# Optimization experiments

Measured on AMD Instinct MI355X. Metric: run time of the kernel, lower is better.

The kernel has to match this reference:

```python
import jax, jax.numpy as jnp
import numpy as np

B = 64
T0_V = 512   # existing timesteps already in the graph memory
TAU_V = 128  # new timesteps inserted this call
NTOT = T0_V + TAU_V  # 640 == graph_size
FEAT = 256
K = 16       # causal temporal window (edges j->i for j in [i-K, i))


def _build_edges():
    # per-batch causal edges, then offset by b*NTOT into the flat graph
    src_l, dst_l = [], []
    for off in range(1, K + 1):
        ii = np.arange(off, NTOT)
        src_l.append(ii - off)
        dst_l.append(ii)
    src = np.concatenate(src_l)
    dst = np.concatenate(dst_l)
    boff = (np.arange(B) * NTOT)[:, None]
    edge_src = (src[None, :] + boff).reshape(-1)
    edge_dst = (dst[None, :] + boff).reshape(-1)
    return jnp.asarray(edge_src, jnp.int32), jnp.asarray(edge_dst, jnp.int32)


def setup_inputs() -> dict:
    key = jax.random.key(0)
    ks = jax.random.split(key, 8)
    x = jax.random.normal(ks[0], (B, TAU_V, FEAT), jnp.float32)
    nodes = 0.1 * jax.random.normal(ks[1], (B, NTOT, FEAT), jnp.float32)
    edge_src, edge_dst = _build_edges()
    E = edge_src.shape[0]
    edge_weight = jnp.ones((E,), jnp.float32)
    sc = 1.0 / np.sqrt(FEAT)
    W1_self = sc * jax.random.normal(ks[2], (FEAT, FEAT), jnp.float32)
    W1_nbr = sc * jax.random.normal(ks[3], (FEAT, FEAT), jnp.float32)
    b1 = jnp.zeros((FEAT,), jnp.float32)
    W2_self = sc * jax.random.normal(ks[4], (FEAT, FEAT), jnp.float32)
    W2_nbr = sc * jax.random.normal(ks[5], (FEAT, FEAT), jnp.float32)
    b2 = jnp.zeros((FEAT,), jnp.float32)
    return {"x": x, "nodes": nodes, "edge_weight": edge_weight,
            "W1_self": W1_self, "W1_nbr": W1_nbr, "b1": b1,
            "W2_self": W2_self, "W2_nbr": W2_nbr, "b2": b2,
            "edge_src": edge_src, "edge_dst": edge_dst,
            "T0": T0_V, "tau": TAU_V}


def reference(x, nodes, edge_weight, W1_self, W1_nbr, b1, W2_self, W2_nbr, b2,
              edge_src, edge_dst, T0, tau):
    Bv, t, feat = x.shape
    ntot = T0 + tau
    # scatter new observations into the node memory (uniform taus -> dense slice)
    nodes = nodes.at[:, T0:T0 + tau, :].set(x)
    # adj normalization: values / values.detach() == 1 in the forward pass
    w = edge_weight / jax.lax.stop_gradient(edge_weight)
    # flatten per-batch ragged graphs (regular here since taus are uniform)
    flat = nodes[:, :ntot].reshape(Bv * ntot, feat)  # [B*ntot, feat]
    nseg = Bv * ntot

    def gconv(h, Ws, Wn, b):
        msg = h[edge_src] * w[:, None]                       # [E, d] gather
        agg = jax.ops.segment_sum(msg, edge_dst, num_segments=nseg)
        return jnp.tanh(h @ Ws + agg @ Wn + b)

    h = gconv(flat, W1_self, W1_nbr, b1)
    h = gconv(h, W2_self, W2_nbr, b2)
    # gather outputs for the newly-inserted nodes -> [B, tau, out_feat]
    out_idx = (jnp.arange(Bv)[:, None] * ntot + T0 + jnp.arange(tau)[None, :]).reshape(-1)
    mx_dense = h[out_idx].reshape(Bv, tau, -1)
    return mx_dense
```

## Files before the change

### kernel.cpp

```cpp
#include <hip/hip_runtime.h>
#include <hip/hip_bf16.h>


namespace {

constexpr int BQ    = 64;
constexpr int FEATC = 256;
constexpr int M1 = 144;
constexpr int M2 = 128;

using ushort = unsigned short;
using short8 = __attribute__((ext_vector_type(8))) short;
using f32x4  = __attribute__((ext_vector_type(4))) float;

__device__ __forceinline__ ushort f2bf(float f) {
  union { float f; unsigned u; } v{f};
  unsigned r = v.u + 0x7FFFu + ((v.u >> 16) & 1u);
  return (ushort)(r >> 16);
}
__device__ __forceinline__ float bf2f(ushort h) {
  union { unsigned u; float f; } v{(unsigned)h << 16};
  return v.f;
}
__device__ __forceinline__ void split2(float v, ushort& hi, ushort& lo) {
  hi = f2bf(v);
  lo = f2bf(v - bf2f(hi));
}
__device__ __forceinline__ float tanh_fast(float x) {
  const float e = __builtin_amdgcn_exp2f(x * 2.8853900817779268f);
  return 1.0f - 2.0f * __builtin_amdgcn_rcpf(1.0f + e);
}

__device__ __forceinline__ size_t frag_idx(int row, int k, int s) {
  return ((size_t)(((row >> 4) * 16 + (k >> 5)) * 2 + s)) * 512
       + ((k >> 3) & 3) * 128 + (row & 15) * 8 + (k & 7);
}
__device__ __forceinline__ int lofs(int row_l, int k, int s) {
  return ((k >> 5) * 2 + s) * 512 + ((k >> 3) & 3) * 128 + row_l * 8 + (k & 7);
}

__global__ __launch_bounds__(256) void prep_fused(
    const float* __restrict__ x, const float* __restrict__ nodes,
    const float* __restrict__ W1s, const float* __restrict__ W1n,
    const float* __restrict__ W2s, const float* __restrict__ W2n,
    ushort* __restrict__ A1F, ushort* __restrict__ WF1,
    ushort* __restrict__ WF2) {
  __shared__ ushort lds_o[16384];
  __shared__ float tile[64][65];
  const int blk = blockIdx.x;
  if (blk < 576) {
    const int G = 4 * (blk % 144) + (blk / 144);
    const int b = G / 9, c = G % 9, f = threadIdx.x;
    const int t0 = c * 16, i0 = 496 + t0;
    const float* nb = nodes + ((size_t)b * 640) * FEATC + f;
    const float* xb = x     + ((size_t)b * 128) * FEATC + f;

    float v[32];
    #pragma unroll
    for (int d = 0; d < 32; ++d) {
      const int i = i0 - 16 + d;
      v[d] = (i < 512) ? nb[(size_t)i * FEATC] : xb[(size_t)(i - 512) * FEATC];
    }
    float win = 0.f;
    #pragma unroll
    for (int d = 0; d < 16; ++d) win += v[d];

    #pragma unroll
    for (int tt = 0; tt < 16; ++tt) {
      ushort hi, lo;
      split2(v[16 + tt], hi, lo);
      lds_o[lofs(tt, f, 0)] = hi;
      lds_o[lofs(tt, f, 1)] = lo;
      split2(win, hi, lo);
      lds_o[lofs(tt, 256 + f, 0)] = hi;
      lds_o[lofs(tt, 256 + f, 1)] = lo;
      win += v[16 + tt] - v[tt];
    }
    __syncthreads();
    ushort* dst = A1F + (size_t)G * 16384;
    #pragma unroll
    for (int it = 0; it < 8; ++it) {
      const int idx = it * 256 + threadIdx.x;
      *(short8*)(dst + idx * 8) = *(const short8*)(lds_o + idx * 8);
    }
  } else {
    const int w = blk - 576;
    const int z = w >> 4, rem = w & 15;
    const int k0 = (rem >> 2) * 64, n0 = (rem & 3) * 64;
    const float* src = (z == 0) ? W1s : (z == 1) ? W1n : (z == 2) ? W2s : W2n;
    ushort* dst = (z < 2) ? WF1 : WF2;
    const int koff = (z & 1) * 256;
    const int c = threadIdx.x & 63, r4 = threadIdx.x >> 6;
    #pragma unroll
    for (int p = 0; p < 16; ++p) {
      const int k = r4 + p * 4;
      tile[k][c] = src[(size_t)(k0 + k) * FEATC + n0 + c];
    }
    __syncthreads();
    #pragma unroll
    for (int p = 0; p < 16; ++p) {
      const int n = r4 + p * 4;
      ushort hi, lo;
      split2(tile[c][n], hi, lo);
      dst[frag_idx(n0 + n, koff + k0 + c, 0)] = hi;
      dst[frag_idx(n0 + n, koff + k0 + c, 1)] = lo;
    }
  }
}

#define GLOAD(dst, ptr)                                                      \
  asm volatile("global_load_dwordx4 %0, %1, off"                             \
               : "=v"(dst) : "v"(ptr) : "memory")

#define WAITV(n) do {                                                        \
  asm volatile("s_waitcnt vmcnt(" #n ")" ::: "memory");                      \
  __builtin_amdgcn_sched_barrier(0);                                         \
} while (0)

#define MF(a, b, c) c = __builtin_amdgcn_mfma_f32_16x16x32_bf16(a, b, c, 0, 0, 0)

struct FJ { short8 a0h, a0l, a1h, a1l, a2h, a2l, a3h, a3l, a4h, a4l, wh, wl; };

#define LOADJ(Q, kb) do {                                                    \
  GLOAD(Q.a0h, bA0 + (kb) * 1024); GLOAD(Q.a0l, bA0 + (kb) * 1024 + 512);    \
  GLOAD(Q.a1h, bA1 + (kb) * 1024); GLOAD(Q.a1l, bA1 + (kb) * 1024 + 512);    \
  GLOAD(Q.a2h, bA2 + (kb) * 1024); GLOAD(Q.a2l, bA2 + (kb) * 1024 + 512);    \
  GLOAD(Q.a3h, bA3 + (kb) * 1024); GLOAD(Q.a3l, bA3 + (kb) * 1024 + 512);    \
  GLOAD(Q.a4h, bA4 + (kb) * 1024); GLOAD(Q.a4l, bA4 + (kb) * 1024 + 512);    \
  GLOAD(Q.wh,  bW  + (kb) * 1024); GLOAD(Q.wl,  bW  + (kb) * 1024 + 512);    \
} while (0)

#define COMPJ(Q) do {                                                        \
  __builtin_amdgcn_s_setprio(1);                                             \
  MF(Q.a0h, Q.wh, acc[0]); MF(Q.a1h, Q.wh, acc[1]); MF(Q.a2h, Q.wh, acc[2]); \
  MF(Q.a3h, Q.wh, acc[3]); MF(Q.a4h, Q.wh, acc[4]);                          \
  MF(Q.a0h, Q.wl, acc[0]); MF(Q.a1h, Q.wl, acc[1]); MF(Q.a2h, Q.wl, acc[2]); \
  MF(Q.a3h, Q.wl, acc[3]); MF(Q.a4h, Q.wl, acc[4]);                          \
  MF(Q.a0l, Q.wh, acc[0]); MF(Q.a1l, Q.wh, acc[1]); MF(Q.a2l, Q.wh, acc[2]); \
  MF(Q.a3l, Q.wh, acc[3]); MF(Q.a4l, Q.wh, acc[4]);                          \
  __builtin_amdgcn_s_setprio(0);                                             \
  __builtin_amdgcn_sched_barrier(0);                                         \
} while (0)

__global__ __launch_bounds__(256, 2) void gemm1_fused(
    const ushort* __restrict__ A, const ushort* __restrict__ W,
    const float* __restrict__ bias, ushort* __restrict__ A2F) {
  __shared__ float hvt[80][68];
  __shared__ ushort outb[16384];

  const int tid = threadIdx.x;
  const int wave = tid >> 6, lane = tid & 63;
  const int lr = lane & 15, kg = lane >> 4;
  const int mx2 = blockIdx.x, ny = blockIdx.y;
  const int b = mx2 >> 1, half = mx2 & 1;
  const int rgA0 = 9 * b + 4 * half;
  const int n0 = ny * 64;
  const int ngw = ny * 4 + wave;

  const ushort* bA0 = A + (size_t)(rgA0 + 0) * 16384 + lane * 8;
  const ushort* bA1 = A + (size_t)(rgA0 + 1) * 16384 + lane * 8;
  const ushort* bA2 = A + (size_t)(rgA0 + 2) * 16384 + lane * 8;
  const ushort* bA3 = A + (size_t)(rgA0 + 3) * 16384 + lane * 8;
  const ushort* bA4 = A + (size_t)(rgA0 + 4) * 16384 + lane * 8;
  const ushort* bW  = W + (size_t)ngw * 16384 + lane * 8;

  f32x4 acc[5] = {};
  FJ q0, q1, q2, q3;

  LOADJ(q0, 0); LOADJ(q1, 1); LOADJ(q2, 2); LOADJ(q3, 3);
  WAITV(36); COMPJ(q0); LOADJ(q0, 4);
  WAITV(36); COMPJ(q1); LOADJ(q1, 5);
  WAITV(36); COMPJ(q2); LOADJ(q2, 6);
  WAITV(36); COMPJ(q3); LOADJ(q3, 7);
  WAITV(36); COMPJ(q0); LOADJ(q0, 8);
  WAITV(36); COMPJ(q1); LOADJ(q1, 9);
  WAITV(36); COMPJ(q2); LOADJ(q2, 10);
  WAITV(36); COMPJ(q3); LOADJ(q3, 11);
  WAITV(36); COMPJ(q0); LOADJ(q0, 12);
  WAITV(36); COMPJ(q1); LOADJ(q1, 13);
  WAITV(36); COMPJ(q2); LOADJ(q2, 14);
  WAITV(36); COMPJ(q3); LOADJ(q3, 15);
  WAITV(36); COMPJ(q0);
  WAITV(24); COMPJ(q1);
  WAITV(12); COMPJ(q2);
  WAITV(0);  COMPJ(q3);

  const float bv = bias[n0 + wave * 16 + lr];
  #pragma unroll
  for (int fr = 0; fr < 5; ++fr)
    #pragma unroll
    for (int r = 0; r < 4; ++r)
      hvt[fr * 16 + kg * 4 + r][wave * 16 + lr] = tanh_fast(acc[fr][r] + bv);
  __syncthreads();

  {
    const int col = tid & 63, q = tid >> 6;
    float hv[32];
    #pragma unroll
    for (int d = 0; d < 32; ++d) hv[d] = hvt[q * 16 + d][col];
    float win = 0.f;
    #pragma unroll
    for (int d = 0; d < 16; ++d) win += hv[d];

    const int su = ((q * 4 + (col >> 5)) * 2) * 512
                 + ((col >> 3) & 3) * 128 + (col & 7);
    const int wu = ((q * 4 + 2 + (col >> 5)) * 2) * 512
                 + ((col >> 3) & 3) * 128 + (col & 7);
    #pragma unroll
    for (int tt = 0; tt < 16; ++tt) {
      ushort hi, lo;
      split2(hv[16 + tt], hi, lo);
      outb[su + tt * 8]       = hi;
      outb[su + tt * 8 + 512] = lo;
      split2(win, hi, lo);
      outb[wu + tt * 8]       = hi;
      outb[wu + tt * 8 + 512] = lo;
      win += hv[16 + tt] - hv[tt];
    }
  }
  __syncthreads();

  const int rg20 = 4 * mx2;
  #pragma unroll
  for (int it = 0; it < 8; ++it) {
    const int lin = it * 2048 + tid * 8;
    const int u = lin >> 9, w = lin & 511;
    const int uq = u >> 3, ukbl = (u >> 1) & 3, us = u & 1;
    const int KB = (ukbl < 2) ? (2 * ny + ukbl) : (8 + 2 * ny + (ukbl - 2));
    const size_t dst = ((size_t)((rg20 + uq) * 16 + KB) * 2 + us) * 512 + w;
    *(short8*)(A2F + dst) = *(const short8*)(outb + lin);
  }
}

struct FB { short8 ah0, ah1, al0, al1, b10, b11, b20, b21; };

#define LOADI(Q, tt) do {                                                    \
  GLOAD(Q.ah0, baseA00 + (tt) * 1024);                                       \
  GLOAD(Q.ah1, baseA10 + (tt) * 1024);                                       \
  GLOAD(Q.al0, baseA01 + (tt) * 1024);                                       \
  GLOAD(Q.al1, baseA11 + (tt) * 1024);                                       \
  GLOAD(Q.b10, baseW0h + (tt) * 1024);                                       \
  GLOAD(Q.b11, baseW1h + (tt) * 1024);                                       \
  GLOAD(Q.b20, baseW0l + (tt) * 1024);                                       \
  GLOAD(Q.b21, baseW1l + (tt) * 1024);                                       \
} while (0)

#define COMP(Q) do {                                                         \
  __builtin_amdgcn_s_setprio(1);                                             \
  MF(Q.ah0, Q.b10, acc00); MF(Q.ah0, Q.b11, acc01);                          \
  MF(Q.ah1, Q.b10, acc10); MF(Q.ah1, Q.b11, acc11);                          \
  MF(Q.ah0, Q.b20, acc00); MF(Q.ah0, Q.b21, acc01);                          \
  MF(Q.ah1, Q.b20, acc10); MF(Q.ah1, Q.b21, acc11);                          \
  MF(Q.al0, Q.b10, acc00); MF(Q.al0, Q.b11, acc01);                          \
  MF(Q.al1, Q.b10, acc10); MF(Q.al1, Q.b11, acc11);                          \
  __builtin_amdgcn_s_setprio(0);                                             \
  __builtin_amdgcn_sched_barrier(0);                                         \
} while (0)

__global__ __launch_bounds__(256, 2) void gemm_mfma(
    const ushort* __restrict__ A, const ushort* __restrict__ W,
    const float* __restrict__ bias, float* __restrict__ out) {
  const int t = threadIdx.x;
  const int wave = t >> 6, lane = t & 63;
  const int lr = lane & 15, kg = lane >> 4;
  const int m0 = blockIdx.x * 64 + (wave >> 1) * 32;
  const int n0 = blockIdx.y * 64 + (wave & 1) * 32;
  const int rg0 = m0 >> 4, ng0 = n0 >> 4;

  const ushort* baseA00 = A + ((size_t)((rg0 + 0) * 32 + 0)) * 512 + lane * 8;
  const ushort* baseA01 = A + ((size_t)((rg0 + 0) * 32 + 1)) * 512 + lane * 8;
  const ushort* baseA10 = A + ((size_t)((rg0 + 1) * 32 + 0)) * 512 + lane * 8;
  const ushort* baseA11 = A + ((size_t)((rg0 + 1) * 32 + 1)) * 512 + lane * 8;
  const ushort* baseW0h = W + ((size_t)((ng0 + 0) * 32 + 0)) * 512 + lane * 8;
  const ushort* baseW0l = W + ((size_t)((ng0 + 0) * 32 + 1)) * 512 + lane * 8;
  const ushort* baseW1h = W + ((size_t)((ng0 + 1) * 32 + 0)) * 512 + lane * 8;
  const ushort* baseW1l = W + ((size_t)((ng0 + 1) * 32 + 1)) * 512 + lane * 8;

  f32x4 acc00 = {}, acc01 = {}, acc10 = {}, acc11 = {};
  FB q0, q1, q2, q3, q4;

  LOADI(q0, 0); LOADI(q1, 1); LOADI(q2, 2); LOADI(q3, 3); LOADI(q4, 4);
  WAITV(32); COMP(q0); LOADI(q0, 5);
  WAITV(32); COMP(q1); LOADI(q1, 6);
  WAITV(32); COMP(q2); LOADI(q2, 7);
  WAITV(32); COMP(q3); LOADI(q3, 8);
  WAITV(32); COMP(q4); LOADI(q4, 9);
  WAITV(32); COMP(q0); LOADI(q0, 10);
  WAITV(32); COMP(q1); LOADI(q1, 11);
  WAITV(32); COMP(q2); LOADI(q2, 12);
  WAITV(32); COMP(q3); LOADI(q3, 13);
  WAITV(32); COMP(q4); LOADI(q4, 14);
  WAITV(32); COMP(q0); LOADI(q0, 15);
  WAITV(32); COMP(q1);
  WAITV(24); COMP(q2);
  WAITV(16); COMP(q3);
  WAITV(8);  COMP(q4);
  WAITV(0);  COMP(q0);

  const float bv0 = bias[n0 + lr];
  const float bv1 = bias[n0 + 16 + lr];
  auto epi = [&](const f32x4& a, int mt, int nt, float bv) {
    #pragma unroll
    for (int r = 0; r < 4; ++r) {
      const int row = m0 + mt * 16 + kg * 4 + r;
      const int col = n0 + nt * 16 + lr;
      out[(size_t)row * FEATC + col] = tanh_fast(a[r] + bv);
    }
  };
  epi(acc00, 0, 0, bv0);
  epi(acc01, 0, 1, bv1);
  epi(acc10, 1, 0, bv0);
  epi(acc11, 1, 1, bv1);
}

}

extern "C" void kernel_launch(void* const* d_in, const int* in_sizes, int n_in,
                              void* d_out, int out_size, void* d_ws, size_t ws_size,
                              hipStream_t stream) {
  const float* x     = (const float*)d_in[0];
  const float* nodes = (const float*)d_in[1];
  const float* W1s = (const float*)d_in[3];
  const float* W1n = (const float*)d_in[4];
  const float* b1  = (const float*)d_in[5];
  const float* W2s = (const float*)d_in[6];
  const float* W2n = (const float*)d_in[7];
  const float* b2  = (const float*)d_in[8];
  float* out = (float*)d_out;

  const size_t a1_sz = (size_t)BQ * M1 * 1024;
  const size_t a2_sz = (size_t)BQ * M2 * 1024;
  const size_t wf_sz = (size_t)16 * 16 * 2 * 512;
  const size_t need = (a1_sz + a2_sz + 2 * wf_sz) * sizeof(ushort);
  if (ws_size < need) return;

  ushort* p = (ushort*)d_ws;
  ushort* A1F = p; p += a1_sz;
  ushort* A2F = p; p += a2_sz;
  ushort* WF1 = p; p += wf_sz;
  ushort* WF2 = p; p += wf_sz;

  prep_fused<<<640, 256, 0, stream>>>(x, nodes, W1s, W1n, W2s, W2n,
                                      A1F, WF1, WF2);
  gemm1_fused<<<dim3(BQ * 2, FEATC / 64), 256, 0, stream>>>(A1F, WF1, b1, A2F);
  gemm_mfma<<<dim3((BQ * M2) / 64, FEATC / 64), 256, 0, stream>>>(
      A2F, WF2, b2, out);
}
```

Before: 41.22 us.

## Stage shared A fragments in LDS via global_load_lds with triple buffering

In gemm1_fused, the A-operand fragments used to be loaded directly into registers by each of the four waves, so every wave fetched the same five A row-groups from global memory. Now the waves split those loads between them and copy the fragments into LDS with async global_load_lds. The loop is triple-buffered and each step ends with a barrier, after which all waves read A from LDS while still loading W directly. This cuts redundant global traffic and register pressure, but adds per-step block barriers, LDS reads and a larger shared-memory footprint that overlaps the epilogue buffers.

```diff
diff --git a/kernel.cpp b/kernel.cpp
--- a/kernel.cpp
+++ b/kernel.cpp
@@ -29,6 +29,11 @@
 __device__ __forceinline__ float tanh_fast(float x) {
   const float e = __builtin_amdgcn_exp2f(x * 2.8853900817779268f);
   return 1.0f - 2.0f * __builtin_amdgcn_rcpf(1.0f + e);
+}
+__device__ __forceinline__ void gl_lds16(const ushort* g, ushort* l) {
+  __builtin_amdgcn_global_load_lds(
+      (const __attribute__((address_space(1))) void*)g,
+      (__attribute__((address_space(3))) void*)l, 16, 0, 0);
 }
 
 __device__ __forceinline__ size_t frag_idx(int row, int k, int s) {
@@ -119,34 +124,44 @@
 
 #define MF(a, b, c) c = __builtin_amdgcn_mfma_f32_16x16x32_bf16(a, b, c, 0, 0, 0)
 
-struct FJ { short8 a0h, a0l, a1h, a1l, a2h, a2l, a3h, a3l, a4h, a4l, wh, wl; };
-
-#define LOADJ(Q, kb) do {                                                    \
-  GLOAD(Q.a0h, bA0 + (kb) * 1024); GLOAD(Q.a0l, bA0 + (kb) * 1024 + 512);    \
-  GLOAD(Q.a1h, bA1 + (kb) * 1024); GLOAD(Q.a1l, bA1 + (kb) * 1024 + 512);    \
-  GLOAD(Q.a2h, bA2 + (kb) * 1024); GLOAD(Q.a2l, bA2 + (kb) * 1024 + 512);    \
-  GLOAD(Q.a3h, bA3 + (kb) * 1024); GLOAD(Q.a3l, bA3 + (kb) * 1024 + 512);    \
-  GLOAD(Q.a4h, bA4 + (kb) * 1024); GLOAD(Q.a4l, bA4 + (kb) * 1024 + 512);    \
-  GLOAD(Q.wh,  bW  + (kb) * 1024); GLOAD(Q.wl,  bW  + (kb) * 1024 + 512);    \
-} while (0)
-
-#define COMPJ(Q) do {                                                        \
-  __builtin_amdgcn_s_setprio(1);                                             \
-  MF(Q.a0h, Q.wh, acc[0]); MF(Q.a1h, Q.wh, acc[1]); MF(Q.a2h, Q.wh, acc[2]); \
-  MF(Q.a3h, Q.wh, acc[3]); MF(Q.a4h, Q.wh, acc[4]);                          \
-  MF(Q.a0h, Q.wl, acc[0]); MF(Q.a1h, Q.wl, acc[1]); MF(Q.a2h, Q.wl, acc[2]); \
-  MF(Q.a3h, Q.wl, acc[3]); MF(Q.a4h, Q.wl, acc[4]);                          \
-  MF(Q.a0l, Q.wh, acc[0]); MF(Q.a1l, Q.wh, acc[1]); MF(Q.a2l, Q.wh, acc[2]); \
-  MF(Q.a3l, Q.wh, acc[3]); MF(Q.a4l, Q.wh, acc[4]);                          \
-  __builtin_amdgcn_s_setprio(0);                                             \
-  __builtin_amdgcn_sched_barrier(0);                                         \
+#define STAGEA(jn, kb) do {                                                  \
+  gl_lds16(srcu0 + (kb) * 1024, sbase + (jn) * 5120 + u0 * 512);             \
+  gl_lds16(srcu1 + (kb) * 1024, sbase + (jn) * 5120 + u1 * 512);             \
+  if (g3) gl_lds16(srcu2 + (kb) * 1024, sbase + (jn) * 5120 + u2 * 512);     \
+} while (0)
+
+#define WAITW do { if (g3) { WAITV(5); } else { WAITV(4); } } while (0)
+
+#define COMPJ2(j, WH, WL) do {                                               \
+  const ushort* bp_ = sbase + (j) * 5120 + lane * 8;                         \
+  const short8 a0h = *(const short8*)(bp_ + 0 * 512);                        \
+  const short8 a0l = *(const short8*)(bp_ + 1 * 512);                        \
+  const short8 a1h = *(const short8*)(bp_ + 2 * 512);                        \
+  const short8 a1l = *(const short8*)(bp_ + 3 * 512);                        \
+  const short8 a2h = *(const short8*)(bp_ + 4 * 512);                        \
+  const short8 a2l = *(const short8*)(bp_ + 5 * 512);                        \
+  const short8 a3h = *(const short8*)(bp_ + 6 * 512);                        \
+  const short8 a3l = *(const short8*)(bp_ + 7 * 512);                        \
+  const short8 a4h = *(const short8*)(bp_ + 8 * 512);                        \
+  const short8 a4l = *(const short8*)(bp_ + 9 * 512);                        \
+  __builtin_amdgcn_s_setprio(1);                                            \
+  MF(a0h, WH, acc[0]); MF(a1h, WH, acc[1]); MF(a2h, WH, acc[2]);             \
+  MF(a3h, WH, acc[3]); MF(a4h, WH, acc[4]);                                  \
+  MF(a0h, WL, acc[0]); MF(a1h, WL, acc[1]); MF(a2h, WL, acc[2]);             \
+  MF(a3h, WL, acc[3]); MF(a4h, WL, acc[4]);                                  \
+  MF(a0l, WH, acc[0]); MF(a1l, WH, acc[1]); MF(a2l, WH, acc[2]);             \
+  MF(a3l, WH, acc[3]); MF(a4l, WH, acc[4]);                                  \
+  __builtin_amdgcn_s_setprio(0);                                            \
+  __builtin_amdgcn_sched_barrier(0);                                        \
 } while (0)
 
 __global__ __launch_bounds__(256, 2) void gemm1_fused(
     const ushort* __restrict__ A, const ushort* __restrict__ W,
     const float* __restrict__ bias, ushort* __restrict__ A2F) {
-  __shared__ float hvt[80][68];
-  __shared__ ushort outb[16384];
+  __shared__ __align__(16) unsigned char ldsmem[54528];
+  ushort* sbase = (ushort*)ldsmem;
+  float (*hvt)[68] = (float(*)[68])ldsmem;
+  ushort* outb = (ushort*)(ldsmem + 21760);
 
   const int tid = threadIdx.x;
   const int wave = tid >> 6, lane = tid & 63;
@@ -157,33 +172,51 @@
   const int n0 = ny * 64;
   const int ngw = ny * 4 + wave;
 
-  const ushort* bA0 = A + (size_t)(rgA0 + 0) * 16384 + lane * 8;
-  const ushort* bA1 = A + (size_t)(rgA0 + 1) * 16384 + lane * 8;
-  const ushort* bA2 = A + (size_t)(rgA0 + 2) * 16384 + lane * 8;
-  const ushort* bA3 = A + (size_t)(rgA0 + 3) * 16384 + lane * 8;
-  const ushort* bA4 = A + (size_t)(rgA0 + 4) * 16384 + lane * 8;
-  const ushort* bW  = W + (size_t)ngw * 16384 + lane * 8;
+  const bool g3 = (wave < 2);
+  const int uw = g3 ? wave * 3 : 6 + (wave - 2) * 2;
+  const int u0 = uw, u1 = uw + 1, u2 = g3 ? uw + 2 : uw + 1;
+  auto srcA = [&](int u) {
+    return A + ((size_t)(rgA0 + (u >> 1)) * 32 + (u & 1)) * 512 + lane * 8;
+  };
+  const ushort* srcu0 = srcA(u0);
+  const ushort* srcu1 = srcA(u1);
+  const ushort* srcu2 = srcA(u2);
+
+  const ushort* bW = W + (size_t)ngw * 16384 + lane * 8;
 
   f32x4 acc[5] = {};
-  FJ q0, q1, q2, q3;
-
-  LOADJ(q0, 0); LOADJ(q1, 1); LOADJ(q2, 2); LOADJ(q3, 3);
-  WAITV(36); COMPJ(q0); LOADJ(q0, 4);
-  WAITV(36); COMPJ(q1); LOADJ(q1, 5);
-  WAITV(36); COMPJ(q2); LOADJ(q2, 6);
-  WAITV(36); COMPJ(q3); LOADJ(q3, 7);
-  WAITV(36); COMPJ(q0); LOADJ(q0, 8);
-  WAITV(36); COMPJ(q1); LOADJ(q1, 9);
-  WAITV(36); COMPJ(q2); LOADJ(q2, 10);
-  WAITV(36); COMPJ(q3); LOADJ(q3, 11);
-  WAITV(36); COMPJ(q0); LOADJ(q0, 12);
-  WAITV(36); COMPJ(q1); LOADJ(q1, 13);
-  WAITV(36); COMPJ(q2); LOADJ(q2, 14);
-  WAITV(36); COMPJ(q3); LOADJ(q3, 15);
-  WAITV(36); COMPJ(q0);
-  WAITV(24); COMPJ(q1);
-  WAITV(12); COMPJ(q2);
-  WAITV(0);  COMPJ(q3);
+  short8 w0h, w0l, w1h, w1l, w2h, w2l;
+
+  STAGEA(0, 0); GLOAD(w0h, bW);        GLOAD(w0l, bW + 512);
+  STAGEA(1, 1); GLOAD(w1h, bW + 1024); GLOAD(w1l, bW + 1536);
+
+#define STEP(k, j, jn, WH, WL, NWH, NWL)                                     \
+  WAITW; __builtin_amdgcn_s_barrier();                                       \
+  COMPJ2(j, WH, WL);                                                         \
+  STAGEA(jn, (k) + 2);                                                       \
+  GLOAD(NWH, bW + ((k) + 2) * 1024); GLOAD(NWL, bW + ((k) + 2) * 1024 + 512)
+
+  STEP(0, 0, 2, w0h, w0l, w2h, w2l);
+  STEP(1, 1, 0, w1h, w1l, w0h, w0l);
+  STEP(2, 2, 1, w2h, w2l, w1h, w1l);
+  STEP(3, 0, 2, w0h, w0l, w2h, w2l);
+  STEP(4, 1, 0, w1h, w1l, w0h, w0l);
+  STEP(5, 2, 1, w2h, w2l, w1h, w1l);
+  STEP(6, 0, 2, w0h, w0l, w2h, w2l);
+  STEP(7, 1, 0, w1h, w1l, w0h, w0l);
+  STEP(8, 2, 1, w2h, w2l, w1h, w1l);
+  STEP(9, 0, 2, w0h, w0l, w2h, w2l);
+  STEP(10, 1, 0, w1h, w1l, w0h, w0l);
+  STEP(11, 2, 1, w2h, w2l, w1h, w1l);
+  STEP(12, 0, 2, w0h, w0l, w2h, w2l);
+  STEP(13, 1, 0, w1h, w1l, w0h, w0l);
+  WAITW; __builtin_amdgcn_s_barrier();
+  COMPJ2(2, w2h, w2l);
+  WAITV(0); __builtin_amdgcn_s_barrier();
+  COMPJ2(0, w0h, w0l);
+#undef STEP
+
+  __syncthreads();
 
   const float bv = bias[n0 + wave * 16 + lr];
   #pragma unroll
```

After: 37.37 us. 9.3% less time.
